# Optimization experiments

Measured on AMD Instinct MI355X. Metric: run time of the kernel, lower is better.

The kernel has to match this reference:

```python
import jax, jax.numpy as jnp
import numpy as np

B, S, IN, OUT = 2, 2048, 4096, 4096


def setup_inputs() -> dict:
    key = jax.random.key(0)
    k1, k2, k3, k4, k5 = jax.random.split(key, 5)
    x = jax.random.normal(k1, (B, S, IN), dtype=jnp.float32)
    weight_int8 = jax.random.randint(k2, (OUT, IN), 0, 127, dtype=jnp.int32)
    weight_scales = jax.random.uniform(k3, (OUT,), dtype=jnp.float32)
    weight_fp = jax.random.normal(k4, (OUT, IN), dtype=jnp.float32) * 0.02
    bias = jax.random.normal(k5, (OUT,), dtype=jnp.float32) * 0.02
    return {"x": x, "weight_int8": weight_int8, "weight_scales": weight_scales,
            "weight_fp": weight_fp, "bias": bias}


def reference(x, weight_int8, weight_scales, weight_fp, bias):
    # Dequantize: per-row scale / 127, cast to activation dtype (matches
    # torch: weight_int8.to(dtype) * (scales.unsqueeze(1)/127).to(dtype)).
    w_dq = weight_int8.astype(x.dtype) * (weight_scales[:, None] / 127.0).astype(x.dtype)
    # out = x @ w_dq.T + bias, over flattened leading dims
    out = jnp.einsum('bsi,oi->bso', x, w_dq) + bias
    return out
```

## Files before the change

kernel.cpp:

```cpp
#include <hip/hip_runtime.h>
#include <hip/hip_bf16.h>
#include <stdint.h>

#define MDIM 4096
#define NDIM 4096
#define KDIM 4096
#define NT   (KDIM / 64)

typedef __attribute__((ext_vector_type(4))) float  f32x4;
typedef __attribute__((ext_vector_type(4))) int    i32x4;
typedef __attribute__((ext_vector_type(8))) short  bf16x8;
typedef __attribute__((ext_vector_type(4))) float  fx4;
typedef __attribute__((ext_vector_type(4))) int    ix4;
typedef __attribute__((ext_vector_type(8))) unsigned short usx8;

__device__ static inline unsigned short f32_to_bf16_rne(float f) {
  union { float f; unsigned int u; } v; v.f = f;
  unsigned int u = v.u;
  u += 0x7fffu + ((u >> 16) & 1u);
  return (unsigned short)(u >> 16);
}

__device__ static inline void gload_lds16(const void* g, void* l) {
  __builtin_amdgcn_global_load_lds((const __attribute__((address_space(1))) void*)g,
                                   (__attribute__((address_space(3))) void*)l,
                                   16, 0, 0);
}

__device__ static inline void mfma_i8(i32x4& d, const i32x4& a, const i32x4& b) {
  asm("v_mfma_i32_16x16x64_i8 %0, %1, %2, %0" : "+v"(d) : "v"(a), "v"(b));
}


__global__ __launch_bounds__(256) void quant_both(
    const float* __restrict__ x, const int* __restrict__ w8,
    signed char* __restrict__ xq, signed char* __restrict__ wq,
    float* __restrict__ xs) {
  const int bid = blockIdx.x, t = threadIdx.x;
  if (bid < MDIM) {
    const float* row = x + (size_t)bid * KDIM + t * 16;
    fx4 v0 = *(const fx4*)(row);
    fx4 v1 = *(const fx4*)(row + 4);
    fx4 v2 = *(const fx4*)(row + 8);
    fx4 v3 = *(const fx4*)(row + 12);
    float am = 0.0f;
#pragma unroll
    for (int j = 0; j < 4; ++j) {
      am = fmaxf(am, fmaxf(__builtin_fabsf(v0[j]), __builtin_fabsf(v1[j])));
      am = fmaxf(am, fmaxf(__builtin_fabsf(v2[j]), __builtin_fabsf(v3[j])));
    }
#pragma unroll
    for (int off = 32; off; off >>= 1) am = fmaxf(am, __shfl_xor(am, off));
    __shared__ float wm[4];
    if ((t & 63) == 0) wm[t >> 6] = am;
    __syncthreads();
    am = fmaxf(fmaxf(wm[0], wm[1]), fmaxf(wm[2], wm[3]));
    am = fmaxf(am, 1e-20f);
    const float qs = 127.0f / am;
    int q[16];
#pragma unroll
    for (int j = 0; j < 4; ++j) {
      q[j]      = (int)rintf(v0[j] * qs);
      q[4 + j]  = (int)rintf(v1[j] * qs);
      q[8 + j]  = (int)rintf(v2[j] * qs);
      q[12 + j] = (int)rintf(v3[j] * qs);
    }
    i32x4 pk;
#pragma unroll
    for (int j = 0; j < 4; ++j)
      pk[j] = (q[4*j] & 255) | ((q[4*j+1] & 255) << 8) |
              ((q[4*j+2] & 255) << 16) | ((q[4*j+3] & 255) << 24);
    *(i32x4*)(xq + (size_t)bid * KDIM + t * 16) = pk;
    if (t == 0) xs[bid] = am * (1.0f / 127.0f);
  } else {
    const int n = bid - MDIM;
    const int* row = w8 + (size_t)n * KDIM + t * 16;
    ix4 w0 = *(const ix4*)(row);
    ix4 w1 = *(const ix4*)(row + 4);
    ix4 w2 = *(const ix4*)(row + 8);
    ix4 w3 = *(const ix4*)(row + 12);
    i32x4 pk;
    pk[0] = (w0[0] & 255) | ((w0[1] & 255) << 8) | ((w0[2] & 255) << 16) | ((w0[3] & 255) << 24);
    pk[1] = (w1[0] & 255) | ((w1[1] & 255) << 8) | ((w1[2] & 255) << 16) | ((w1[3] & 255) << 24);
    pk[2] = (w2[0] & 255) | ((w2[1] & 255) << 8) | ((w2[2] & 255) << 16) | ((w2[3] & 255) << 24);
    pk[3] = (w3[0] & 255) | ((w3[1] & 255) << 8) | ((w3[2] & 255) << 16) | ((w3[3] & 255) << 24);
    *(i32x4*)(wq + (size_t)n * KDIM + t * 16) = pk;
  }
}


__global__ __launch_bounds__(512, 2) void gemm_i8(
    const signed char* __restrict__ Aq,
    const signed char* __restrict__ Wq,
    const float* __restrict__ xs,
    const float* __restrict__ scales,
    const float* __restrict__ bias,
    float* __restrict__ C) {
  __shared__ signed char Ash[2 * 16384];
  __shared__ signed char Bsh[2 * 16384];

  const int tid = threadIdx.x;
  const int w   = tid >> 6;
  const int l   = tid & 63;
  const int wr  = w >> 2;
  const int wc  = w & 3;
  const int fr  = l & 15;
  const int fq  = l >> 4;

  const int id  = blockIdx.x;
  const int swz = (id & 7) * 32 + (id >> 3);
  const int bm  = swz >> 4, bn = swz & 15;

  const signed char* aorg = Aq + (size_t)(bm * 256) * KDIM;
  const signed char* borg = Wq + (size_t)(bn * 256) * KDIM;

  const int lr = l >> 2;
  const int ks = (l & 3) ^ ((l >> 3) & 3);
  const size_t g_off = (size_t)(w * 16 + lr) * KDIM + (size_t)ks * 16;
  const int    s_off = w * 1024;

#define STAGE(isB, t, h) do {                                                   \
    const signed char* _g = ((isB) ? borg : aorg)                               \
        + (size_t)(h) * 128 * KDIM + (size_t)(t) * 64 + g_off;                  \
    signed char* _l = ((isB) ? Bsh : Ash)                                       \
        + (((t) & 1) * 16384 + (h) * 8192 + s_off);                             \
    gload_lds16(_g, _l);                                                        \
  } while (0)

  const int arow = (wr * 128 + fr) * 64;
  const int brow = (wc * 64  + fr) * 64;
  const int sl   = (fq ^ ((fr >> 1) & 3)) * 16;

#define LDA(off, rb) (*(const i32x4*)(Ash + (off) + arow + (rb) * 1024 + sl))
#define LDB(off, nc) (*(const i32x4*)(Bsh + (off) + brow + (nc) * 1024 + sl))

#define BAR   __builtin_amdgcn_s_barrier()
#define LGKM0 asm volatile("s_waitcnt lgkmcnt(0)" ::: "memory")
#define VM4   asm volatile("s_waitcnt vmcnt(4)" ::: "memory")
#define VM0   asm volatile("s_waitcnt vmcnt(0)" ::: "memory")
#define NOVM  ((void)0)
#define SP1   __builtin_amdgcn_s_setprio(1)
#define SP0   __builtin_amdgcn_s_setprio(0)

  i32x4 acc[8][4] = {};
  i32x4 a0[4], a1[4], b0[2], b1[2];

#define READ_A0(CO) { _Pragma("unroll") for (int rb = 0; rb < 4; ++rb) a0[rb] = LDA(CO, rb); }
#define READ_A1(CO) { _Pragma("unroll") for (int rb = 0; rb < 4; ++rb) a1[rb] = LDA(CO, 4 + rb); }
#define READ_B0(CO) { _Pragma("unroll") for (int cb = 0; cb < 2; ++cb) b0[cb] = LDB(CO, cb); }
#define READ_B1(CO) { _Pragma("unroll") for (int cb = 0; cb < 2; ++cb) b1[cb] = LDB(CO, 2 + cb); }

#define MFMA_Q(MH, NH, AA, BB)                                                  \
  { _Pragma("unroll") for (int rb = 0; rb < 4; ++rb)                            \
    _Pragma("unroll") for (int cb = 0; cb < 2; ++cb)                            \
      mfma_i8(acc[(MH)*4+rb][(NH)*2+cb], AA[rb], BB[cb]); }

#define TILE(U, CO, NX, S2, VMST) do {                                          \
    const int _nx = (CO) ^ 16384;                                               \
                               \
    READ_B1(CO); READ_A1(CO);                                                   \
    SP1; MFMA_Q(0, 0, a0, b0); MFMA_Q(0, 1, a0, b1); SP0;                       \
    LGKM0; BAR;                                                                 \
                         \
    if (S2) { STAGE(0, (U) + 2, 0); STAGE(0, (U) + 2, 1);                       \
              STAGE(1, (U) + 2, 0); STAGE(1, (U) + 2, 1); }                     \
    SP1; MFMA_Q(1, 0, a1, b0); MFMA_Q(1, 1, a1, b1); SP0;                       \
    VMST; BAR;                                                                  \
    if (NX) { READ_A0(_nx); READ_B0(_nx); }                                     \
  } while (0)

  STAGE(0, 0, 0); STAGE(0, 0, 1); STAGE(1, 0, 0); STAGE(1, 0, 1);
  STAGE(0, 1, 0); STAGE(0, 1, 1); STAGE(1, 1, 0); STAGE(1, 1, 1);
  VM4;
  BAR;
  READ_A0(0); READ_B0(0);

#pragma unroll 2
  for (int u = 0; u < NT - 2; ++u) {
    const int cur = (u & 1) * 16384;
    TILE(u, cur, 1, 1, VM4);
  }
  TILE(NT - 2, 0,     1, 0, VM0);
  TILE(NT - 1, 16384, 0, 0, NOVM);

#undef TILE
#undef MFMA_Q
#undef READ_A0
#undef READ_A1
#undef READ_B0
#undef READ_B1
#undef STAGE
#undef LDA
#undef LDB

  const float inv127 = 1.0f / 127.0f;
  const int n_base = bn * 256 + wc * 64;
  const int m_base = bm * 256 + wr * 128 + fq * 4;
  float xr[8][4];
#pragma unroll
  for (int rb = 0; rb < 8; ++rb)
#pragma unroll
    for (int r = 0; r < 4; ++r) xr[rb][r] = xs[m_base + rb * 16 + r];
#pragma unroll
  for (int nc = 0; nc < 4; ++nc) {
    const int n = n_base + nc * 16 + fr;
    const float sw = scales[n] * inv127;
    const float bz = bias[n];
#pragma unroll
    for (int rb = 0; rb < 8; ++rb) {
      float* cp = C + (size_t)(m_base + rb * 16) * NDIM + n;
#pragma unroll
      for (int r = 0; r < 4; ++r)
        cp[(size_t)r * NDIM] = (float)acc[rb][nc][r] * (xr[rb][r] * sw) + bz;
    }
  }
}


__global__ __launch_bounds__(256) void gemm_fused(
    const float* __restrict__ X,
    const int* __restrict__ W,
    const float* __restrict__ scales,
    const float* __restrict__ bias,
    float* __restrict__ C) {
  __shared__ unsigned short As[128 * 32];
  __shared__ unsigned short Bs[128 * 32];

  const int tid = threadIdx.x;
  const int lane = tid & 63;
  const int wave = tid >> 6;
  const int wr = wave >> 1, wc = wave & 1;
  const int fr = lane & 15, fq = lane >> 4;

  int id = blockIdx.x;
  int swz = (id & 7) * 128 + (id >> 3);
  const int bm = swz >> 5, bn = swz & 31;

  const int r0 = tid >> 2;
  const int kc = (tid & 3) * 8;
  const size_t aBase = (size_t)(bm * 128 + r0) * KDIM + kc;
  const size_t bBase = (size_t)(bn * 128 + r0) * KDIM + kc;

  f32x4 acc[4][4] = {};

  for (int k0 = 0; k0 < KDIM; k0 += 32) {
    const float* xp = X + aBase + k0;
    const int*   wp = W + bBase + k0;
    fx4 x0 = *(const fx4*)xp;
    fx4 x1 = *(const fx4*)(xp + 4);
    fx4 x2 = *(const fx4*)(xp + (size_t)64 * KDIM);
    fx4 x3 = *(const fx4*)(xp + (size_t)64 * KDIM + 4);
    ix4 w0 = *(const ix4*)wp;
    ix4 w1 = *(const ix4*)(wp + 4);
    ix4 w2 = *(const ix4*)(wp + (size_t)64 * KDIM);
    ix4 w3 = *(const ix4*)(wp + (size_t)64 * KDIM + 4);

    usx8 ca, cb, cc, cd;
#pragma unroll
    for (int j = 0; j < 4; ++j) {
      ca[j] = f32_to_bf16_rne(x0[j]);  ca[j + 4] = f32_to_bf16_rne(x1[j]);
      cb[j] = f32_to_bf16_rne(x2[j]);  cb[j + 4] = f32_to_bf16_rne(x3[j]);
      cc[j] = f32_to_bf16_rne((float)w0[j]); cc[j + 4] = f32_to_bf16_rne((float)w1[j]);
      cd[j] = f32_to_bf16_rne((float)w2[j]); cd[j + 4] = f32_to_bf16_rne((float)w3[j]);
    }

    __syncthreads();
    *reinterpret_cast<usx8*>(As + tid * 8)        = ca;
    *reinterpret_cast<usx8*>(As + 2048 + tid * 8) = cb;
    *reinterpret_cast<usx8*>(Bs + tid * 8)        = cc;
    *reinterpret_cast<usx8*>(Bs + 2048 + tid * 8) = cd;
    __syncthreads();

    bf16x8 af[4], bfr[4];
    const unsigned short* ap = As + (wr * 64 + fr) * 32 + fq * 8;
    const unsigned short* bp = Bs + (wc * 64 + fr) * 32 + fq * 8;
#pragma unroll
    for (int i = 0; i < 4; ++i) {
      af[i]  = *reinterpret_cast<const bf16x8*>(ap + i * 512);
      bfr[i] = *reinterpret_cast<const bf16x8*>(bp + i * 512);
    }
#pragma unroll
    for (int im = 0; im < 4; ++im)
#pragma unroll
      for (int in_ = 0; in_ < 4; ++in_)
        acc[im][in_] = __builtin_amdgcn_mfma_f32_16x16x32_bf16(
            af[im], bfr[in_], acc[im][in_], 0, 0, 0);
  }

  const float inv127 = 1.0f / 127.0f;
#pragma unroll
  for (int in_ = 0; in_ < 4; ++in_) {
    int n = bn * 128 + wc * 64 + in_ * 16 + fr;
    float sc = scales[n] * inv127;
    float bz = bias[n];
#pragma unroll
    for (int im = 0; im < 4; ++im) {
      int m0 = bm * 128 + wr * 64 + im * 16 + fq * 4;
      float* cp = C + (size_t)m0 * NDIM + n;
#pragma unroll
      for (int r = 0; r < 4; ++r)
        cp[(size_t)r * NDIM] = acc[im][in_][r] * sc + bz;
    }
  }
}


extern "C" void kernel_launch(void* const* d_in, const int* in_sizes, int n_in,
                              void* d_out, int out_size, void* d_ws, size_t ws_size,
                              hipStream_t stream) {
  const float* x      = (const float*)d_in[0];
  const int*   w8     = (const int*)d_in[1];
  const float* scales = (const float*)d_in[2];
  const float* bias   = (const float*)d_in[4];
  float* out = (float*)d_out;

  const size_t xq_bytes = (size_t)MDIM * KDIM;
  const size_t wq_bytes = (size_t)NDIM * KDIM;
  const size_t xs_bytes = (size_t)MDIM * sizeof(float);
  const size_t need = xq_bytes + wq_bytes + xs_bytes;

  if (ws_size >= need) {
    signed char* xq = (signed char*)d_ws;
    signed char* wq = xq + xq_bytes;
    float*       xs = (float*)(wq + wq_bytes);
    quant_both<<<MDIM + NDIM, 256, 0, stream>>>(x, w8, xq, wq, xs);
    gemm_i8<<<256, 512, 0, stream>>>(xq, wq, xs, scales, bias, out);
  } else {
    gemm_fused<<<1024, 256, 0, stream>>>(x, w8, scales, bias, out);
  }
}
```

Before: 95.20 us.

## Shrink int8 GEMM tile to 128x128 with simpler double-buffered loop

Reworks the int8 GEMM from 256x256 tiles with 512 threads and an interleaved split-phase pipeline to 128x128 tiles with 256 threads and a simple double-buffered K loop, launching 1024 blocks. This raises the block count and occupancy and simplifies scheduling. In exchange it lowers data reuse per tile and waits on all outstanding global loads each iteration. It also removes the priority hints and the overlap of LDS reads with MFMA.

```diff
diff --git a/kernel.cpp b/kernel.cpp
--- a/kernel.cpp
+++ b/kernel.cpp
@@ -89,129 +89,100 @@
 }
 
 
-__global__ __launch_bounds__(512, 2) void gemm_i8(
+__global__ __launch_bounds__(256, 4) void gemm_i8(
     const signed char* __restrict__ Aq,
     const signed char* __restrict__ Wq,
     const float* __restrict__ xs,
     const float* __restrict__ scales,
     const float* __restrict__ bias,
     float* __restrict__ C) {
-  __shared__ signed char Ash[2 * 16384];
-  __shared__ signed char Bsh[2 * 16384];
+  __shared__ signed char Ash[2 * 8192];
+  __shared__ signed char Bsh[2 * 8192];
 
   const int tid = threadIdx.x;
   const int w   = tid >> 6;
   const int l   = tid & 63;
-  const int wr  = w >> 2;
-  const int wc  = w & 3;
+  const int wr  = w >> 1;
+  const int wc  = w & 1;
   const int fr  = l & 15;
   const int fq  = l >> 4;
 
   const int id  = blockIdx.x;
-  const int swz = (id & 7) * 32 + (id >> 3);
-  const int bm  = swz >> 4, bn = swz & 15;
-
-  const signed char* aorg = Aq + (size_t)(bm * 256) * KDIM;
-  const signed char* borg = Wq + (size_t)(bn * 256) * KDIM;
-
-  const int lr = l >> 2;
+  const int swz = (id & 7) * 128 + (id >> 3);
+  const int bm  = swz >> 5, bn = swz & 31;
+
+  const signed char* aorg = Aq + (size_t)(bm * 128) * KDIM;
+  const signed char* borg = Wq + (size_t)(bn * 128) * KDIM;
+
   const int ks = (l & 3) ^ ((l >> 3) & 3);
-  const size_t g_off = (size_t)(w * 16 + lr) * KDIM + (size_t)ks * 16;
+  const size_t g_off = (size_t)(w * 16 + (l >> 2)) * KDIM + (size_t)ks * 16;
   const int    s_off = w * 1024;
 
-#define STAGE(isB, t, h) do {                                                   \
+#define STAGE(isB, t, P, h) do {                                                \
     const signed char* _g = ((isB) ? borg : aorg)                               \
-        + (size_t)(h) * 128 * KDIM + (size_t)(t) * 64 + g_off;                  \
-    signed char* _l = ((isB) ? Bsh : Ash)                                       \
-        + (((t) & 1) * 16384 + (h) * 8192 + s_off);                             \
+        + (size_t)(h) * 64 * KDIM + (size_t)(t) * 64 + g_off;                   \
+    signed char* _l = ((isB) ? Bsh : Ash) + ((P) + (h) * 4096 + s_off);         \
     gload_lds16(_g, _l);                                                        \
   } while (0)
 
-  const int arow = (wr * 128 + fr) * 64;
-  const int brow = (wc * 64  + fr) * 64;
-  const int sl   = (fq ^ ((fr >> 1) & 3)) * 16;
-
-#define LDA(off, rb) (*(const i32x4*)(Ash + (off) + arow + (rb) * 1024 + sl))
-#define LDB(off, nc) (*(const i32x4*)(Bsh + (off) + brow + (nc) * 1024 + sl))
+  const int sl    = (fq ^ ((fr >> 1) & 3)) * 16;
+  const int abase = (wr * 64 + fr) * 64 + sl;
+  const int bbase = (wc * 64 + fr) * 64 + sl;
 
 #define BAR   __builtin_amdgcn_s_barrier()
 #define LGKM0 asm volatile("s_waitcnt lgkmcnt(0)" ::: "memory")
-#define VM4   asm volatile("s_waitcnt vmcnt(4)" ::: "memory")
 #define VM0   asm volatile("s_waitcnt vmcnt(0)" ::: "memory")
-#define NOVM  ((void)0)
-#define SP1   __builtin_amdgcn_s_setprio(1)
-#define SP0   __builtin_amdgcn_s_setprio(0)
-
-  i32x4 acc[8][4] = {};
-  i32x4 a0[4], a1[4], b0[2], b1[2];
-
-#define READ_A0(CO) { _Pragma("unroll") for (int rb = 0; rb < 4; ++rb) a0[rb] = LDA(CO, rb); }
-#define READ_A1(CO) { _Pragma("unroll") for (int rb = 0; rb < 4; ++rb) a1[rb] = LDA(CO, 4 + rb); }
-#define READ_B0(CO) { _Pragma("unroll") for (int cb = 0; cb < 2; ++cb) b0[cb] = LDB(CO, cb); }
-#define READ_B1(CO) { _Pragma("unroll") for (int cb = 0; cb < 2; ++cb) b1[cb] = LDB(CO, 2 + cb); }
-
-#define MFMA_Q(MH, NH, AA, BB)                                                  \
-  { _Pragma("unroll") for (int rb = 0; rb < 4; ++rb)                            \
-    _Pragma("unroll") for (int cb = 0; cb < 2; ++cb)                            \
-      mfma_i8(acc[(MH)*4+rb][(NH)*2+cb], AA[rb], BB[cb]); }
-
-#define TILE(U, CO, NX, S2, VMST) do {                                          \
-    const int _nx = (CO) ^ 16384;                                               \
-                               \
-    READ_B1(CO); READ_A1(CO);                                                   \
-    SP1; MFMA_Q(0, 0, a0, b0); MFMA_Q(0, 1, a0, b1); SP0;                       \
-    LGKM0; BAR;                                                                 \
-                         \
-    if (S2) { STAGE(0, (U) + 2, 0); STAGE(0, (U) + 2, 1);                       \
-              STAGE(1, (U) + 2, 0); STAGE(1, (U) + 2, 1); }                     \
-    SP1; MFMA_Q(1, 0, a1, b0); MFMA_Q(1, 1, a1, b1); SP0;                       \
-    VMST; BAR;                                                                  \
-    if (NX) { READ_A0(_nx); READ_B0(_nx); }                                     \
-  } while (0)
-
-  STAGE(0, 0, 0); STAGE(0, 0, 1); STAGE(1, 0, 0); STAGE(1, 0, 1);
-  STAGE(0, 1, 0); STAGE(0, 1, 1); STAGE(1, 1, 0); STAGE(1, 1, 1);
-  VM4;
+
+  i32x4 acc[4][4] = {};
+  i32x4 a[4], b[4];
+
+  STAGE(0, 0, 0, 0); STAGE(0, 0, 0, 1); STAGE(1, 0, 0, 0); STAGE(1, 0, 0, 1);
+  VM0;
   BAR;
-  READ_A0(0); READ_B0(0);
 
 #pragma unroll 2
-  for (int u = 0; u < NT - 2; ++u) {
-    const int cur = (u & 1) * 16384;
-    TILE(u, cur, 1, 1, VM4);
-  }
-  TILE(NT - 2, 0,     1, 0, VM0);
-  TILE(NT - 1, 16384, 0, 0, NOVM);
-
-#undef TILE
-#undef MFMA_Q
-#undef READ_A0
-#undef READ_A1
-#undef READ_B0
-#undef READ_B1
+  for (int u = 0; u < NT; ++u) {
+    const int cp = (u & 1) * 8192;
+    const int np = cp ^ 8192;
+    if (u + 1 < NT) {
+      STAGE(0, u + 1, np, 0); STAGE(0, u + 1, np, 1);
+      STAGE(1, u + 1, np, 0); STAGE(1, u + 1, np, 1);
+    }
+#pragma unroll
+    for (int rb = 0; rb < 4; ++rb) a[rb] = *(const i32x4*)(Ash + cp + abase + rb * 1024);
+#pragma unroll
+    for (int cb = 0; cb < 4; ++cb) b[cb] = *(const i32x4*)(Bsh + cp + bbase + cb * 1024);
+#pragma unroll
+    for (int rb = 0; rb < 4; ++rb)
+#pragma unroll
+      for (int cb = 0; cb < 4; ++cb)
+        mfma_i8(acc[rb][cb], a[rb], b[cb]);
+    LGKM0;
+    VM0;
+    BAR;
+  }
+
 #undef STAGE
-#undef LDA
-#undef LDB
 
   const float inv127 = 1.0f / 127.0f;
-  const int n_base = bn * 256 + wc * 64;
-  const int m_base = bm * 256 + wr * 128 + fq * 4;
-  float xr[8][4];
-#pragma unroll
-  for (int rb = 0; rb < 8; ++rb)
+  const int m_base = bm * 128 + wr * 64 + fq * 4;
+  const int n_base = bn * 128 + wc * 64;
+  float xr[4][4];
+#pragma unroll
+  for (int rb = 0; rb < 4; ++rb)
 #pragma unroll
     for (int r = 0; r < 4; ++r) xr[rb][r] = xs[m_base + rb * 16 + r];
 #pragma unroll
-  for (int nc = 0; nc < 4; ++nc) {
-    const int n = n_base + nc * 16 + fr;
+  for (int cb = 0; cb < 4; ++cb) {
+    const int n = n_base + cb * 16 + fr;
     const float sw = scales[n] * inv127;
     const float bz = bias[n];
 #pragma unroll
-    for (int rb = 0; rb < 8; ++rb) {
+    for (int rb = 0; rb < 4; ++rb) {
       float* cp = C + (size_t)(m_base + rb * 16) * NDIM + n;
 #pragma unroll
       for (int r = 0; r < 4; ++r)
-        cp[(size_t)r * NDIM] = (float)acc[rb][nc][r] * (xr[rb][r] * sw) + bz;
+        cp[(size_t)r * NDIM] = (float)acc[rb][cb][r] * (xr[rb][r] * sw) + bz;
     }
   }
 }
@@ -324,7 +295,7 @@
     signed char* wq = xq + xq_bytes;
     float*       xs = (float*)(wq + wq_bytes);
     quant_both<<<MDIM + NDIM, 256, 0, stream>>>(x, w8, xq, wq, xs);
-    gemm_i8<<<256, 512, 0, stream>>>(xq, wq, xs, scales, bias, out);
+    gemm_i8<<<1024, 256, 0, stream>>>(xq, wq, xs, scales, bias, out);
   } else {
     gemm_fused<<<1024, 256, 0, stream>>>(x, w8, scales, bias, out);
   }
```

Result: slower. 110.2 us (+15.8%).

## Switch int8 GEMM LDS pipeline to triple buffering with one barrier per tile

Applied to the files above, without the earlier changes.

Grows the shared-memory A/B staging buffers from two stages to three and rotates them across an unrolled-by-3 main loop. Global-to-LDS loads for tile u+2 are now issued at the start of each tile, and all 32 MFMAs run back to back, so each tile needs one barrier instead of two. This is meant to cut synchronisation stalls and overlap loads with compute better. The cost is LDS rising from 64 KB to 96 KB per block, which may not allow two 512-thread blocks per CU under the launch bounds and could lower occupancy.

```diff
diff --git a/kernel.cpp b/kernel.cpp
--- a/kernel.cpp
+++ b/kernel.cpp
@@ -96,8 +96,8 @@
     const float* __restrict__ scales,
     const float* __restrict__ bias,
     float* __restrict__ C) {
-  __shared__ signed char Ash[2 * 16384];
-  __shared__ signed char Bsh[2 * 16384];
+  __shared__ signed char Ash[3 * 16384];
+  __shared__ signed char Bsh[3 * 16384];
 
   const int tid = threadIdx.x;
   const int w   = tid >> 6;
@@ -119,11 +119,10 @@
   const size_t g_off = (size_t)(w * 16 + lr) * KDIM + (size_t)ks * 16;
   const int    s_off = w * 1024;
 
-#define STAGE(isB, t, h) do {                                                   \
+#define STAGE(isB, t, h, P) do {                                                \
     const signed char* _g = ((isB) ? borg : aorg)                               \
         + (size_t)(h) * 128 * KDIM + (size_t)(t) * 64 + g_off;                  \
-    signed char* _l = ((isB) ? Bsh : Ash)                                       \
-        + (((t) & 1) * 16384 + (h) * 8192 + s_off);                             \
+    signed char* _l = ((isB) ? Bsh : Ash) + ((P) + (h) * 8192 + s_off);         \
     gload_lds16(_g, _l);                                                        \
   } while (0)
 
@@ -134,13 +133,17 @@
 #define LDA(off, rb) (*(const i32x4*)(Ash + (off) + arow + (rb) * 1024 + sl))
 #define LDB(off, nc) (*(const i32x4*)(Bsh + (off) + brow + (nc) * 1024 + sl))
 
-#define BAR   __builtin_amdgcn_s_barrier()
-#define LGKM0 asm volatile("s_waitcnt lgkmcnt(0)" ::: "memory")
-#define VM4   asm volatile("s_waitcnt vmcnt(4)" ::: "memory")
-#define VM0   asm volatile("s_waitcnt vmcnt(0)" ::: "memory")
-#define NOVM  ((void)0)
-#define SP1   __builtin_amdgcn_s_setprio(1)
-#define SP0   __builtin_amdgcn_s_setprio(0)
+#define BAR    __builtin_amdgcn_s_barrier()
+#define SCHED0 __builtin_amdgcn_sched_barrier(0)
+#define VM4    asm volatile("s_waitcnt vmcnt(4)" ::: "memory")
+#define VM0    asm volatile("s_waitcnt vmcnt(0)" ::: "memory")
+#define NOVM   ((void)0)
+#define SP1    __builtin_amdgcn_s_setprio(1)
+#define SP0    __builtin_amdgcn_s_setprio(0)
+
+#define B0OF 0
+#define B1OF 16384
+#define B2OF 32768
 
   i32x4 acc[8][4] = {};
   i32x4 a0[4], a1[4], b0[2], b1[2];
@@ -155,33 +158,39 @@
     _Pragma("unroll") for (int cb = 0; cb < 2; ++cb)                            \
       mfma_i8(acc[(MH)*4+rb][(NH)*2+cb], AA[rb], BB[cb]); }
 
-#define TILE(U, CO, NX, S2, VMST) do {                                          \
-    const int _nx = (CO) ^ 16384;                                               \
-                               \
-    READ_B1(CO); READ_A1(CO);                                                   \
-    SP1; MFMA_Q(0, 0, a0, b0); MFMA_Q(0, 1, a0, b1); SP0;                       \
-    LGKM0; BAR;                                                                 \
-                         \
-    if (S2) { STAGE(0, (U) + 2, 0); STAGE(0, (U) + 2, 1);                       \
-              STAGE(1, (U) + 2, 0); STAGE(1, (U) + 2, 1); }                     \
-    SP1; MFMA_Q(1, 0, a1, b0); MFMA_Q(1, 1, a1, b1); SP0;                       \
-    VMST; BAR;                                                                  \
-    if (NX) { READ_A0(_nx); READ_B0(_nx); }                                     \
+#define TILE(U, CUR, STG, NXT, S2, VMST, NX) do {                               \
+    if (S2) { STAGE(0, (U) + 2, 0, STG); STAGE(0, (U) + 2, 1, STG);             \
+              STAGE(1, (U) + 2, 0, STG); STAGE(1, (U) + 2, 1, STG); }           \
+    READ_B1(CUR); READ_A1(CUR);                                                 \
+    SP1;                                                                        \
+    MFMA_Q(0, 0, a0, b0);              \
+    MFMA_Q(0, 1, a0, b1);                                                       \
+    MFMA_Q(1, 0, a1, b0);                                                       \
+    MFMA_Q(1, 1, a1, b1);                                                       \
+    SP0;                                                                        \
+    VMST; BAR; SCHED0;                                                          \
+    if (NX) { READ_A0(NXT); READ_B0(NXT); }                                     \
   } while (0)
 
-  STAGE(0, 0, 0); STAGE(0, 0, 1); STAGE(1, 0, 0); STAGE(1, 0, 1);
-  STAGE(0, 1, 0); STAGE(0, 1, 1); STAGE(1, 1, 0); STAGE(1, 1, 1);
+  STAGE(0, 0, 0, B0OF); STAGE(0, 0, 1, B0OF);
+  STAGE(1, 0, 0, B0OF); STAGE(1, 0, 1, B0OF);
+  STAGE(0, 1, 0, B1OF); STAGE(0, 1, 1, B1OF);
+  STAGE(1, 1, 0, B1OF); STAGE(1, 1, 1, B1OF);
   VM4;
-  BAR;
-  READ_A0(0); READ_B0(0);
-
-#pragma unroll 2
-  for (int u = 0; u < NT - 2; ++u) {
-    const int cur = (u & 1) * 16384;
-    TILE(u, cur, 1, 1, VM4);
-  }
-  TILE(NT - 2, 0,     1, 0, VM0);
-  TILE(NT - 1, 16384, 0, 0, NOVM);
+  BAR; SCHED0;
+  READ_A0(B0OF); READ_B0(B0OF);
+
+#pragma unroll 1
+  for (int i = 0; i < 20; ++i) {
+    const int u0 = 3 * i;
+    TILE(u0,     B0OF, B2OF, B1OF, 1, VM4, 1);
+    TILE(u0 + 1, B1OF, B0OF, B2OF, 1, VM4, 1);
+    TILE(u0 + 2, B2OF, B1OF, B0OF, 1, VM4, 1);
+  }
+  TILE(60, B0OF, B2OF, B1OF, 1, VM4,  1);
+  TILE(61, B1OF, B0OF, B2OF, 1, VM4,  1);
+  TILE(62, B2OF, B1OF, B0OF, 0, VM0,  1);
+  TILE(63, B0OF, B1OF, B2OF, 0, NOVM, 0);
 
 #undef TILE
 #undef MFMA_Q
```

Result: no change. 96.39 us (+1.2%).
